# Optimization experiments

Hardware: AMD Instinct MI355X
Metric: run time of the kernel (lower is better)

## Reference

```python
import jax, jax.numpy as jnp
import numpy as np

H, I, E, K = 1024, 2816, 8, 2  # hidden, intermediate, n_experts, topk
B, S = 2, 2048


def setup_inputs() -> dict:
    key = jax.random.key(0)
    ks = jax.random.split(key, 6)
    def init(k, shape, fan_in):
        return (jax.random.normal(k, shape, jnp.float32) / np.sqrt(fan_in)).astype(jnp.float32)
    return {
        "x": jax.random.normal(ks[0], (B, S, H), jnp.float32),
        "Wgate": init(ks[1], (H, E), H),   # gating Linear weight (in,out layout)
        "bgate": jnp.zeros((E,), jnp.float32),  # gating Linear bias (nn.Linear default bias=True)
        "Wg": init(ks[2], (E, H, I), H),   # stacked gate_proj, mlp_bias=False
        "Wu": init(ks[3], (E, H, I), H),   # stacked up_proj
        "Wd": init(ks[4], (E, I, H), I),   # stacked down_proj
    }


def reference(x, Wgate, bgate, Wg, Wu, Wd):
    Bb, Ss, Hd = x.shape
    xf = x.reshape(-1, Hd)                       # [N, H] flattened tokens
    logits = xf @ Wgate + bgate                  # [N, E] gate logits
    topv, topi = jax.lax.top_k(logits, K)        # [N, K]
    N = xf.shape[0]
    # sparse combine weights: raw top-k LOGITS (no softmax), zeros elsewhere
    # (faithful to torch: scatter of logits_topk into -inf mask; -inf slots
    #  are never read since only selected experts contribute)
    combine = jnp.zeros_like(logits).at[jnp.arange(N)[:, None], topi].set(topv)  # [N, E]
    # dense grouped SwiGLU over all experts, then sparse combine
    g = jnp.einsum('nh,ehi->nei', xf, Wg)        # [N, E, I]
    u = jnp.einsum('nh,ehi->nei', xf, Wu)        # [N, E, I]
    h = jax.nn.silu(g) * u                       # [N, E, I]
    eo = jnp.einsum('nei,eih->neh', h, Wd)       # [N, E, H]
    out = jnp.einsum('neh,ne->nh', eo, combine).reshape(Bb, Ss, Hd)
    return out, logits
```

## Files before the change

kernel.cpp:

```cpp
#include <hip/hip_runtime.h>

#define HDIM 1024
#define IDIM 2816
#define NEXP 8
#define NTOK 4096
#define NROWS 8192
#define RPAD 8320
#define MAXT 71
#define GU_NYT 44
#define GU_TG 8
#define GU_NTG 9
#define GU_NWG (GU_NTG * GU_NYT * GU_TG)
#define DN_NWG 576
#define TLDP 66
#define N_TGU 5632
#define N_GATE 1024

typedef short bf16x8 __attribute__((ext_vector_type(8)));
typedef float f32x4 __attribute__((ext_vector_type(4)));
typedef unsigned short u16x8 __attribute__((ext_vector_type(8)));

static __device__ __forceinline__ float bf2f(unsigned int u) {
    union { unsigned int i; float f; } v; v.i = u << 16; return v.f;
}
static __device__ __forceinline__ unsigned short f2bf(float f) {
    union { float f; unsigned int i; } v; v.f = f;
    return (unsigned short)((v.i + 0x7fffu + ((v.i >> 16) & 1u)) >> 16);
}

static __device__ __forceinline__ void gload16(const void* g, void* l) {
    __builtin_amdgcn_global_load_lds(
        (const __attribute__((address_space(1))) unsigned int*)g,
        (__attribute__((address_space(3))) unsigned int*)l, 16, 0, 0);
}

static __device__ __forceinline__ void tp_read_tile64(
    const float* __restrict__ sp, int C, int tid, unsigned short* lds)
{
#pragma unroll
    for (int q = 0; q < 8; ++q) {
        int idx = q * 1024 + tid * 4;
        int r = idx >> 6, cc = idx & 63;
        float4 v = *reinterpret_cast<const float4*>(sp + (size_t)r * C + cc);
        unsigned w0 = (unsigned)f2bf(v.x) | ((unsigned)f2bf(v.y) << 16);
        unsigned w1 = (unsigned)f2bf(v.z) | ((unsigned)f2bf(v.w) << 16);
        unsigned* lp = reinterpret_cast<unsigned*>(&lds[r * TLDP + cc]);
        lp[0] = w0; lp[1] = w1;
    }
}

__global__ __launch_bounds__(256) void prep_kernel(
    const float* __restrict__ Wg, const float* __restrict__ Wu,
    unsigned short* __restrict__ W2,
    const float* __restrict__ x, const float* __restrict__ Wgate,
    const float* __restrict__ bgate, float* __restrict__ logits_out,
    int* __restrict__ counts, int* __restrict__ topi, float* __restrict__ topv)
{
    __shared__ unsigned short lds[128 * TLDP];
    const int b = blockIdx.x;
    const int tid = threadIdx.x;

    if (b < N_TGU) {
        const int kind = b / (NEXP * 352);
        const int rem = b % (NEXP * 352);
        const int e = rem / 352;
        const int tt = rem % 352;
        const int tr = tt / 44, tc = tt % 44;

        const float* s0 = (kind ? Wu : Wg) + (size_t)e * HDIM * IDIM;
        tp_read_tile64(s0 + (size_t)(tr * 128) * IDIM + tc * 64, IDIM, tid, lds);
        __syncthreads();
        const int g = tid & 15;
        unsigned short* d0 = W2 + (size_t)e * 2 * IDIM * HDIM + tr * 128 + g * 8;
#pragma unroll
        for (int cb = 0; cb < 4; ++cb) {
            int c = cb * 16 + (tid >> 4);
            u16x8 o;
#pragma unroll
            for (int jj = 0; jj < 8; ++jj) o[jj] = lds[(g * 8 + jj) * TLDP + c];
            int i = tc * 64 + c;
            int r2 = ((i >> 4) << 5) + (kind << 4) + (i & 15);
            *reinterpret_cast<u16x8*>(d0 + (size_t)r2 * HDIM) = o;
        }
        return;
    }

    int bb = b - N_TGU;
    int wave = (bb << 2) + (tid >> 6);
    int lane = tid & 63;
    if (wave >= NTOK) return;
    const float* xr = x + (size_t)wave * HDIM;

    double acc[NEXP];
#pragma unroll
    for (int e = 0; e < NEXP; ++e) acc[e] = 0.0;
    for (int it = 0; it < HDIM / 64; ++it) {
        int h = lane + (it << 6);
        float xv = xr[h];
        const float* wr = Wgate + (size_t)h * NEXP;
#pragma unroll
        for (int e = 0; e < NEXP; ++e) acc[e] += (double)xv * (double)wr[e];
    }
#pragma unroll
    for (int e = 0; e < NEXP; ++e) {
        double v = acc[e];
        for (int off = 32; off; off >>= 1) v += __shfl_xor(v, off, 64);
        acc[e] = v + (double)bgate[e];
    }
    float lf[NEXP];
#pragma unroll
    for (int e = 0; e < NEXP; ++e) lf[e] = (float)acc[e];

    if (lane < NEXP) logits_out[(size_t)wave * NEXP + lane] = lf[lane];

    if (lane == 0) {
        int i1 = 0; float v1 = lf[0];
#pragma unroll
        for (int e = 1; e < NEXP; ++e) if (lf[e] > v1) { v1 = lf[e]; i1 = e; }
        int i2 = -1; float v2 = -3.0e38f;
#pragma unroll
        for (int e = 0; e < NEXP; ++e) {
            if (e == i1) continue;
            if (lf[e] > v2) { v2 = lf[e]; i2 = e; }
        }
        topi[wave * 2 + 0] = i1; topv[wave * 2 + 0] = v1;
        topi[wave * 2 + 1] = i2; topv[wave * 2 + 1] = v2;
        atomicAdd(&counts[i1], 1);
        atomicAdd(&counts[i2], 1);
    }
}

__global__ void offsets_kernel(const int* __restrict__ counts,
                               int* __restrict__ offs, int* __restrict__ cursor,
                               int* __restrict__ ntile, int* __restrict__ te,
                               int* __restrict__ tm0)
{
    if (threadIdx.x == 0 && blockIdx.x == 0) {
        int s = 0;
        for (int e = 0; e < NEXP; ++e) { offs[e] = s; cursor[e] = s; s += counts[e]; }
        offs[NEXP] = s;
        int nt = 0;
        for (int e = 0; e < NEXP; ++e) {
            int c = counts[e], base = offs[e];
            for (int mt = 0; mt * 128 < c; ++mt) { te[nt] = e; tm0[nt] = base + mt * 128; ++nt; }
        }
        *ntile = nt;
    }
}

__global__ __launch_bounds__(256) void scatter_kernel(
    const float* __restrict__ x, const int* __restrict__ topi,
    const float* __restrict__ topv, int* __restrict__ cursor,
    float* __restrict__ row_w, int* __restrict__ pos_of,
    unsigned short* __restrict__ Xg)
{
    int p = (blockIdx.x << 2) + (threadIdx.x >> 6);
    int lane = threadIdx.x & 63;
    if (p >= NROWS) return;
    int n = p >> 1;
    int e = topi[p];
    float w = topv[p];
    int pos = 0;
    if (lane == 0) {
        pos = atomicAdd(&cursor[e], 1);
        row_w[pos] = w;
        pos_of[p] = pos;
    }
    pos = __shfl(pos, 0, 64);
    const float* xr = x + (size_t)n * HDIM;
    unsigned short* dst = Xg + (size_t)pos * HDIM;
#pragma unroll
    for (int it = 0; it < HDIM / 256; ++it) {
        int idx = (it * 64 + lane) * 4;
        float4 v = *reinterpret_cast<const float4*>(&xr[idx]);
        ushort4 o;
        o.x = f2bf(v.x); o.y = f2bf(v.y); o.z = f2bf(v.z); o.w = f2bf(v.w);
        *reinterpret_cast<ushort4*>(&dst[idx]) = o;
    }
}

__global__ __launch_bounds__(256) void transpose_d_kernel(
    const float* __restrict__ Wd, unsigned short* __restrict__ Wdt)
{
    __shared__ unsigned short lds[128 * TLDP];
    const int e = blockIdx.y;
    const int tt = blockIdx.x;
    const int tr = tt / 16, tc = tt % 16;
    const int tid = threadIdx.x;

    const float* s0 = Wd + (size_t)e * IDIM * HDIM;
    tp_read_tile64(s0 + (size_t)(tr * 128) * HDIM + tc * 64, HDIM, tid, lds);
    __syncthreads();
    {
        const int g = tid & 15;
        unsigned short* d0 = Wdt + (size_t)e * HDIM * IDIM + tr * 128 + g * 8;
#pragma unroll
        for (int cb = 0; cb < 4; ++cb) {
            int c = cb * 16 + (tid >> 4);
            u16x8 o;
#pragma unroll
            for (int jj = 0; jj < 8; ++jj) o[jj] = lds[(g * 8 + jj) * TLDP + c];
            *reinterpret_cast<u16x8*>(d0 + (size_t)(tc * 64 + c) * IDIM) = o;
        }
    }
}

__global__ __launch_bounds__(256, 4) void gateup_kernel(
    const unsigned short* __restrict__ Xg,
    const unsigned short* __restrict__ W2,
    const int* __restrict__ offs,
    const int* __restrict__ ntile, const int* __restrict__ te,
    const int* __restrict__ tm0, unsigned short* __restrict__ hbuf)
{
    __shared__ unsigned short As[128 * 64];
    __shared__ unsigned short Bs[128 * 64];

    int bid = blockIdx.x;
    int xcd = bid & 7, rest = bid >> 3;
    int wg = xcd * (GU_NWG / 8) + rest;
    int tg = wg / (GU_NYT * GU_TG);
    int r2 = wg % (GU_NYT * GU_TG);
    int ny = r2 >> 3, ti = r2 & 7;
    int t = tg * GU_TG + ti;
    if (t >= *ntile) return;

    const int e = te[t];
    const int m0 = tm0[t];
    const int r1 = offs[e + 1];
    const int n0 = ny * 128;

    const unsigned short* wb = W2 + (size_t)e * 2 * IDIM * HDIM;

    const int tid = threadIdx.x;
    const int lane = tid & 63, wv = tid >> 6;
    const int wr = (wv >> 1) * 64, wc = (wv & 1) * 64;
    const int lr = lane & 15, kq16 = lane >> 4;

    const int a_row8 = tid >> 3;
    const int a_c16 = tid & 7;

    f32x4 acc[4][4];
#pragma unroll
    for (int m = 0; m < 4; ++m)
#pragma unroll
        for (int n = 0; n < 4; ++n) acc[m][n] = {0.f, 0.f, 0.f, 0.f};

    for (int k0 = 0; k0 < HDIM; k0 += 64) {
        __syncthreads();
#pragma unroll
        for (int ch = 0; ch < 4; ++ch) {
            int row = ch * 32 + a_row8;
            int c16s = a_c16 ^ (row & 7);
            gload16(&Xg[(size_t)(m0 + row) * HDIM + k0 + c16s * 8], &As[ch * 2048 + tid * 8]);
            gload16(&wb[(size_t)(n0 + row) * HDIM + k0 + c16s * 8], &Bs[ch * 2048 + tid * 8]);
        }
        __syncthreads();

#pragma unroll
        for (int ks = 0; ks < 2; ++ks) {
            bf16x8 af[4], bf[4];
#pragma unroll
            for (int m = 0; m < 4; ++m) {
                int row = wr + m * 16 + lr;
                int sw = (ks * 4 + kq16) ^ (row & 7);
                af[m] = *reinterpret_cast<const bf16x8*>(&As[row * 64 + sw * 8]);
            }
#pragma unroll
            for (int n = 0; n < 4; ++n) {
                int row = wc + n * 16 + lr;
                int sw = (ks * 4 + kq16) ^ (row & 7);
                bf[n] = *reinterpret_cast<const bf16x8*>(&Bs[row * 64 + sw * 8]);
            }
#pragma unroll
            for (int m = 0; m < 4; ++m)
#pragma unroll
                for (int n = 0; n < 4; ++n)
                    acc[m][n] = __builtin_amdgcn_mfma_f32_16x16x32_bf16(af[m], bf[n], acc[m][n], 0, 0, 0);
        }
    }

    const int rr = (lane >> 4) * 4;
    const int iloc0 = ((wc >> 5) << 4) + lr;
    const int col0 = ny * 64 + iloc0;
#pragma unroll
    for (int m = 0; m < 4; ++m) {
#pragma unroll
        for (int j = 0; j < 4; ++j) {
            int grow = m0 + wr + m * 16 + rr + j;
            if (grow < r1) {
                unsigned short* hr = &hbuf[(size_t)grow * IDIM + col0];
                float g0 = acc[m][0][j], u0 = acc[m][1][j];
                float g1 = acc[m][2][j], u1 = acc[m][3][j];
                hr[0]  = f2bf(g0 / (1.0f + __expf(-g0)) * u0);
                hr[16] = f2bf(g1 / (1.0f + __expf(-g1)) * u1);
            }
        }
    }
}

__global__ __launch_bounds__(256, 4) void down_kernel(
    const unsigned short* __restrict__ hbuf,
    const unsigned short* __restrict__ Wdt,
    const int* __restrict__ offs,
    const int* __restrict__ ntile, const int* __restrict__ te,
    const int* __restrict__ tm0,
    const float* __restrict__ row_w,
    unsigned short* __restrict__ eobuf)
{
    __shared__ unsigned short As[128 * 64];
    __shared__ unsigned short Bs[128 * 64];

    int bid = blockIdx.x;
    int xcd = bid & 7, rest = bid >> 3;
    int tg = rest >> 3, ny = rest & 7;
    int t = xcd * 9 + tg;
    if (t >= *ntile) return;

    const int e = te[t];
    const int m0 = tm0[t];
    const int r1 = offs[e + 1];
    const int n0 = ny * 128;

    const unsigned short* wd = Wdt + (size_t)e * HDIM * IDIM;

    const int tid = threadIdx.x;
    const int lane = tid & 63, wv = tid >> 6;
    const int wr = (wv >> 1) * 64, wc = (wv & 1) * 64;
    const int lr = lane & 15, kq16 = lane >> 4;

    const int a_row8 = tid >> 3;
    const int a_c16 = tid & 7;

    f32x4 acc[4][4];
#pragma unroll
    for (int m = 0; m < 4; ++m)
#pragma unroll
        for (int n = 0; n < 4; ++n) acc[m][n] = {0.f, 0.f, 0.f, 0.f};

    for (int k0 = 0; k0 < IDIM; k0 += 64) {
        __syncthreads();
#pragma unroll
        for (int ch = 0; ch < 4; ++ch) {
            int row = ch * 32 + a_row8;
            int c16s = a_c16 ^ (row & 7);
            gload16(&hbuf[(size_t)(m0 + row) * IDIM + k0 + c16s * 8], &As[ch * 2048 + tid * 8]);
            gload16(&wd[(size_t)(n0 + row) * IDIM + k0 + c16s * 8], &Bs[ch * 2048 + tid * 8]);
        }
        __syncthreads();

#pragma unroll
        for (int ks = 0; ks < 2; ++ks) {
            bf16x8 af[4], bf[4];
#pragma unroll
            for (int m = 0; m < 4; ++m) {
                int row = wr + m * 16 + lr;
                int sw = (ks * 4 + kq16) ^ (row & 7);
                af[m] = *reinterpret_cast<const bf16x8*>(&As[row * 64 + sw * 8]);
            }
#pragma unroll
            for (int n = 0; n < 4; ++n) {
                int row = wc + n * 16 + lr;
                int sw = (ks * 4 + kq16) ^ (row & 7);
                bf[n] = *reinterpret_cast<const bf16x8*>(&Bs[row * 64 + sw * 8]);
            }
#pragma unroll
            for (int m = 0; m < 4; ++m)
#pragma unroll
                for (int n = 0; n < 4; ++n)
                    acc[m][n] = __builtin_amdgcn_mfma_f32_16x16x32_bf16(af[m], bf[n], acc[m][n], 0, 0, 0);
        }
    }

    const int rr = (lane >> 4) * 4;
#pragma unroll
    for (int m = 0; m < 4; ++m) {
#pragma unroll
        for (int j = 0; j < 4; ++j) {
            int grow = m0 + wr + m * 16 + rr + j;
            if (grow < r1) {
                float w = row_w[grow];
                unsigned short* er = &eobuf[(size_t)grow * HDIM + n0 + wc + lr];
#pragma unroll
                for (int n = 0; n < 4; ++n)
                    er[n * 16] = f2bf(acc[m][n][j] * w);
            }
        }
    }
}

__global__ __launch_bounds__(256) void combine_kernel(
    const unsigned short* __restrict__ eobuf, const int* __restrict__ pos_of,
    float* __restrict__ out)
{
    int t = blockIdx.x * 256 + threadIdx.x;
    int n = t >> 7;
    int c = (t & 127) << 3;
    int p0 = pos_of[n * 2 + 0];
    int p1 = pos_of[n * 2 + 1];
    uint4 a = *reinterpret_cast<const uint4*>(&eobuf[(size_t)p0 * HDIM + c]);
    uint4 b = *reinterpret_cast<const uint4*>(&eobuf[(size_t)p1 * HDIM + c]);
    float4 o0, o1;
    o0.x = bf2f(a.x & 0xffffu) + bf2f(b.x & 0xffffu);
    o0.y = bf2f(a.x >> 16)     + bf2f(b.x >> 16);
    o0.z = bf2f(a.y & 0xffffu) + bf2f(b.y & 0xffffu);
    o0.w = bf2f(a.y >> 16)     + bf2f(b.y >> 16);
    o1.x = bf2f(a.z & 0xffffu) + bf2f(b.z & 0xffffu);
    o1.y = bf2f(a.z >> 16)     + bf2f(b.z >> 16);
    o1.z = bf2f(a.w & 0xffffu) + bf2f(b.w & 0xffffu);
    o1.w = bf2f(a.w >> 16)     + bf2f(b.w >> 16);
    float* op = out + (size_t)n * HDIM + c;
    *reinterpret_cast<float4*>(op) = o0;
    *reinterpret_cast<float4*>(op + 4) = o1;
}

extern "C" void kernel_launch(void* const* d_in, const int* in_sizes, int n_in,
                              void* d_out, int out_size, void* d_ws, size_t ws_size,
                              hipStream_t stream)
{
    const float* x     = (const float*)d_in[0];
    const float* Wgate = (const float*)d_in[1];
    const float* bgate = (const float*)d_in[2];
    const float* Wg    = (const float*)d_in[3];
    const float* Wu    = (const float*)d_in[4];
    const float* Wd    = (const float*)d_in[5];
    float* out = (float*)d_out;
    float* logits = out + (size_t)NTOK * HDIM;

    char* ws = (char*)d_ws;
    unsigned short* Xg   = (unsigned short*)ws;
    unsigned short* hbuf = (unsigned short*)(ws + 17039360);
    unsigned short* W2   = (unsigned short*)(ws + 63897600);
    char* meta = ws + 156172288;
    int*   counts  = (int*)(meta);
    int*   offs    = (int*)(meta + 64);
    int*   cursor  = (int*)(meta + 128);
    int*   ntile   = (int*)(meta + 192);
    int*   te      = (int*)(meta + 256);
    int*   tm0     = (int*)(meta + 768);
    int*   topi    = (int*)(meta + 4096);
    float* topv    = (float*)(meta + 36864);
    float* row_w   = (float*)(meta + 69632);
    int*   pos_of  = (int*)(meta + 102400);

    hipMemsetAsync(counts, 0, 32, stream);

    prep_kernel<<<N_TGU + N_GATE, 256, 0, stream>>>(
        Wg, Wu, W2, x, Wgate, bgate, logits, counts, topi, topv);

    offsets_kernel<<<1, 64, 0, stream>>>(counts, offs, cursor, ntile, te, tm0);
    scatter_kernel<<<NROWS / 4, 256, 0, stream>>>(x, topi, topv, cursor, row_w, pos_of, Xg);

    gateup_kernel<<<GU_NWG, 256, 0, stream>>>(Xg, W2, offs, ntile, te, tm0, hbuf);

    transpose_d_kernel<<<dim3(352, NEXP), 256, 0, stream>>>(Wd, W2);

    down_kernel<<<DN_NWG, 256, 0, stream>>>(hbuf, W2, offs, ntile, te, tm0,
                                            row_w, Xg );

    combine_kernel<<<NTOK * HDIM / 8 / 256, 256, 0, stream>>>(Xg, pos_of, out);
}
```

Measured before the change: 457.5 us.

## Fuse gate/up weight fp32-to-bf16 transpose into gateup GEMM B-tile load

Removes the separate pre-pass that converted and transposed Wg/Wu into a bf16 interleaved buffer. The gateup kernel now reads fp32 weights directly, converts pairs with v_cvt_pk_bf16_f32, and writes them swizzled into a padded LDS B tile. This avoids writing and re-reading about 92MB of bf16 weights. In exchange, each tile re-reads fp32 weights (twice the bytes per tile, once per M-tile), does conversion work in the GEMM loop, and uses register-staged loads instead of async global-to-LDS copies.

Measured after the change: 552.2 us. +20.7%, slower.

```diff
diff --git a/kernel.cpp b/kernel.cpp
--- a/kernel.cpp
+++ b/kernel.cpp
@@ -13,8 +13,7 @@
 #define GU_NWG (GU_NTG * GU_NYT * GU_TG)
 #define DN_NWG 576
 #define TLDP 66
-#define N_TGU 5632
-#define N_GATE 1024
+#define BLDP 68
 
 typedef short bf16x8 __attribute__((ext_vector_type(8)));
 typedef float f32x4 __attribute__((ext_vector_type(4)));
@@ -34,60 +33,13 @@
         (__attribute__((address_space(3))) unsigned int*)l, 16, 0, 0);
 }
 
-static __device__ __forceinline__ void tp_read_tile64(
-    const float* __restrict__ sp, int C, int tid, unsigned short* lds)
-{
-#pragma unroll
-    for (int q = 0; q < 8; ++q) {
-        int idx = q * 1024 + tid * 4;
-        int r = idx >> 6, cc = idx & 63;
-        float4 v = *reinterpret_cast<const float4*>(sp + (size_t)r * C + cc);
-        unsigned w0 = (unsigned)f2bf(v.x) | ((unsigned)f2bf(v.y) << 16);
-        unsigned w1 = (unsigned)f2bf(v.z) | ((unsigned)f2bf(v.w) << 16);
-        unsigned* lp = reinterpret_cast<unsigned*>(&lds[r * TLDP + cc]);
-        lp[0] = w0; lp[1] = w1;
-    }
-}
-
-__global__ __launch_bounds__(256) void prep_kernel(
-    const float* __restrict__ Wg, const float* __restrict__ Wu,
-    unsigned short* __restrict__ W2,
+__global__ __launch_bounds__(256) void gating_kernel(
     const float* __restrict__ x, const float* __restrict__ Wgate,
     const float* __restrict__ bgate, float* __restrict__ logits_out,
     int* __restrict__ counts, int* __restrict__ topi, float* __restrict__ topv)
 {
-    __shared__ unsigned short lds[128 * TLDP];
-    const int b = blockIdx.x;
-    const int tid = threadIdx.x;
-
-    if (b < N_TGU) {
-        const int kind = b / (NEXP * 352);
-        const int rem = b % (NEXP * 352);
-        const int e = rem / 352;
-        const int tt = rem % 352;
-        const int tr = tt / 44, tc = tt % 44;
-
-        const float* s0 = (kind ? Wu : Wg) + (size_t)e * HDIM * IDIM;
-        tp_read_tile64(s0 + (size_t)(tr * 128) * IDIM + tc * 64, IDIM, tid, lds);
-        __syncthreads();
-        const int g = tid & 15;
-        unsigned short* d0 = W2 + (size_t)e * 2 * IDIM * HDIM + tr * 128 + g * 8;
-#pragma unroll
-        for (int cb = 0; cb < 4; ++cb) {
-            int c = cb * 16 + (tid >> 4);
-            u16x8 o;
-#pragma unroll
-            for (int jj = 0; jj < 8; ++jj) o[jj] = lds[(g * 8 + jj) * TLDP + c];
-            int i = tc * 64 + c;
-            int r2 = ((i >> 4) << 5) + (kind << 4) + (i & 15);
-            *reinterpret_cast<u16x8*>(d0 + (size_t)r2 * HDIM) = o;
-        }
-        return;
-    }
-
-    int bb = b - N_TGU;
-    int wave = (bb << 2) + (tid >> 6);
-    int lane = tid & 63;
+    int wave = (blockIdx.x << 2) + (threadIdx.x >> 6);
+    int lane = threadIdx.x & 63;
     if (wave >= NTOK) return;
     const float* xr = x + (size_t)wave * HDIM;
 
@@ -179,6 +131,21 @@
     }
 }
 
+static __device__ __forceinline__ void tp_read_tile64(
+    const float* __restrict__ sp, int C, int tid, unsigned short* lds)
+{
+#pragma unroll
+    for (int q = 0; q < 8; ++q) {
+        int idx = q * 1024 + tid * 4;
+        int r = idx >> 6, cc = idx & 63;
+        float4 v = *reinterpret_cast<const float4*>(sp + (size_t)r * C + cc);
+        unsigned w0 = (unsigned)f2bf(v.x) | ((unsigned)f2bf(v.y) << 16);
+        unsigned w1 = (unsigned)f2bf(v.z) | ((unsigned)f2bf(v.w) << 16);
+        unsigned* lp = reinterpret_cast<unsigned*>(&lds[r * TLDP + cc]);
+        lp[0] = w0; lp[1] = w1;
+    }
+}
+
 __global__ __launch_bounds__(256) void transpose_d_kernel(
     const float* __restrict__ Wd, unsigned short* __restrict__ Wdt)
 {
@@ -207,13 +174,13 @@
 
 __global__ __launch_bounds__(256, 4) void gateup_kernel(
     const unsigned short* __restrict__ Xg,
-    const unsigned short* __restrict__ W2,
+    const float* __restrict__ Wg, const float* __restrict__ Wu,
     const int* __restrict__ offs,
     const int* __restrict__ ntile, const int* __restrict__ te,
     const int* __restrict__ tm0, unsigned short* __restrict__ hbuf)
 {
     __shared__ unsigned short As[128 * 64];
-    __shared__ unsigned short Bs[128 * 64];
+    __shared__ unsigned short Bs[128 * BLDP];
 
     int bid = blockIdx.x;
     int xcd = bid & 7, rest = bid >> 3;
@@ -227,9 +194,10 @@
     const int e = te[t];
     const int m0 = tm0[t];
     const int r1 = offs[e + 1];
-    const int n0 = ny * 128;
-
-    const unsigned short* wb = W2 + (size_t)e * 2 * IDIM * HDIM;
+    const int i0 = ny * 64;
+
+    const float* wgp = Wg + (size_t)e * HDIM * IDIM;
+    const float* wup = Wu + (size_t)e * HDIM * IDIM;
 
     const int tid = threadIdx.x;
     const int lane = tid & 63, wv = tid >> 6;
@@ -247,12 +215,39 @@
 
     for (int k0 = 0; k0 < HDIM; k0 += 64) {
         __syncthreads();
+        float4 va[4], vb[4];
+#pragma unroll
+        for (int p = 0; p < 4; ++p) {
+            int v = p * 256 + tid;
+            int iq = v & 15, kd = (v >> 4) & 1, hp = v >> 5;
+            const float* sp = (kd ? wup : wgp) + (size_t)(k0 + hp * 2) * IDIM + i0 + iq * 4;
+            va[p] = *reinterpret_cast<const float4*>(sp);
+            vb[p] = *reinterpret_cast<const float4*>(sp + IDIM);
+        }
 #pragma unroll
         for (int ch = 0; ch < 4; ++ch) {
             int row = ch * 32 + a_row8;
             int c16s = a_c16 ^ (row & 7);
             gload16(&Xg[(size_t)(m0 + row) * HDIM + k0 + c16s * 8], &As[ch * 2048 + tid * 8]);
-            gload16(&wb[(size_t)(n0 + row) * HDIM + k0 + c16s * 8], &Bs[ch * 2048 + tid * 8]);
+        }
+#pragma unroll
+        for (int p = 0; p < 4; ++p) {
+            int v = p * 256 + tid;
+            int iq = v & 15, kd = (v >> 4) & 1, hp = v >> 5;
+            int ioff = iq * 4;
+            int nbase = ((ioff >> 4) << 5) + (kd << 4) + (ioff & 15);
+            int k = hp * 2;
+            int kc = k >> 3, klo = k & 7;
+            const float* fa = reinterpret_cast<const float*>(&va[p]);
+            const float* fb = reinterpret_cast<const float*>(&vb[p]);
+#pragma unroll
+            for (int j = 0; j < 4; ++j) {
+                int n = nbase + j;
+                int sw = kc ^ (n & 7);
+                unsigned pk;
+                asm("v_cvt_pk_bf16_f32 %0, %1, %2" : "=v"(pk) : "v"(fa[j]), "v"(fb[j]));
+                *reinterpret_cast<unsigned*>(&Bs[n * BLDP + sw * 8 + klo]) = pk;
+            }
         }
         __syncthreads();
 
@@ -269,7 +264,7 @@
             for (int n = 0; n < 4; ++n) {
                 int row = wc + n * 16 + lr;
                 int sw = (ks * 4 + kq16) ^ (row & 7);
-                bf[n] = *reinterpret_cast<const bf16x8*>(&Bs[row * 64 + sw * 8]);
+                bf[n] = *reinterpret_cast<const bf16x8*>(&Bs[row * BLDP + sw * 8]);
             }
 #pragma unroll
             for (int m = 0; m < 4; ++m)
@@ -429,7 +424,7 @@
     char* ws = (char*)d_ws;
     unsigned short* Xg   = (unsigned short*)ws;
     unsigned short* hbuf = (unsigned short*)(ws + 17039360);
-    unsigned short* W2   = (unsigned short*)(ws + 63897600);
+    unsigned short* Wdt  = (unsigned short*)(ws + 63897600);
     char* meta = ws + 156172288;
     int*   counts  = (int*)(meta);
     int*   offs    = (int*)(meta + 64);
@@ -444,17 +439,15 @@
 
     hipMemsetAsync(counts, 0, 32, stream);
 
-    prep_kernel<<<N_TGU + N_GATE, 256, 0, stream>>>(
-        Wg, Wu, W2, x, Wgate, bgate, logits, counts, topi, topv);
-
+    gating_kernel<<<NTOK / 4, 256, 0, stream>>>(x, Wgate, bgate, logits, counts, topi, topv);
     offsets_kernel<<<1, 64, 0, stream>>>(counts, offs, cursor, ntile, te, tm0);
     scatter_kernel<<<NROWS / 4, 256, 0, stream>>>(x, topi, topv, cursor, row_w, pos_of, Xg);
 
-    gateup_kernel<<<GU_NWG, 256, 0, stream>>>(Xg, W2, offs, ntile, te, tm0, hbuf);
-
-    transpose_d_kernel<<<dim3(352, NEXP), 256, 0, stream>>>(Wd, W2);
-
-    down_kernel<<<DN_NWG, 256, 0, stream>>>(hbuf, W2, offs, ntile, te, tm0,
+    gateup_kernel<<<GU_NWG, 256, 0, stream>>>(Xg, Wg, Wu, offs, ntile, te, tm0, hbuf);
+
+    transpose_d_kernel<<<dim3(352, NEXP), 256, 0, stream>>>(Wd, Wdt);
+
+    down_kernel<<<DN_NWG, 256, 0, stream>>>(hbuf, Wdt, offs, ntile, te, tm0,
                                             row_w, Xg );
 
     combine_kernel<<<NTOK * HDIM / 8 / 256, 256, 0, stream>>>(Xg, pos_of, out);
```
